# Optimization experiments

Measured on AMD Instinct MI355X. Metric: run time of the kernel, lower is better.

The kernel has to match this reference:

```python
import jax, jax.numpy as jnp
import numpy as np

# ---- configuration (matches init_kwargs) ----
CONTROL_BITS = 8
DATA_BITS = 256          # output_units
STATE_UNITS = 512        # hidden_state_dim
NUM_HEADS = 4
NUM_SHIFT = 3            # odd, required by circular conv
M = 32                   # memory content size (slots per address)
N_ADDR = 256             # memory_addresses_size
SEQ_LEN = 256
BATCH = 64
IN_DIM = CONTROL_BITS + DATA_BITS
READ_SIZE = NUM_HEADS * M
# per-head interface params: s(shift), jd(1), j(3), gamma(1), erase(M), add(M), k(M), beta(1), g(1)
PARAM_SIZES = [NUM_SHIFT, 1, 3, 1, M, M, M, 1, 1]
CUM = np.cumsum([0] + PARAM_SIZES).tolist()
HEAD_PARAM = CUM[-1]
UPDATE_SIZE = NUM_HEADS * HEAD_PARAM
COMB = IN_DIM + STATE_UNITS + READ_SIZE
EPS = 1e-12


def setup_inputs() -> dict:
    key = jax.random.key(0)
    ks = jax.random.split(key, 4)
    def lin(k, fi, fo):
        return (jax.random.normal(k, (fi, fo), jnp.float32) / np.sqrt(fi).astype(np.float32))
    return {
        "inputs": jax.random.normal(ks[0], (BATCH, SEQ_LEN, IN_DIM), jnp.float32),
        "Wo": lin(ks[1], COMB, DATA_BITS), "bo": jnp.zeros((DATA_BITS,), jnp.float32),
        "Ws": lin(ks[2], COMB, STATE_UNITS), "bs": jnp.zeros((STATE_UNITS,), jnp.float32),
        "Wu": lin(ks[3], COMB, UPDATE_SIZE), "bu": jnp.zeros((UPDATE_SIZE,), jnp.float32),
    }


def _circular_conv(x, f):
    # x: [B,H,N], f: [B,H,S] (S odd). y[i] = sum_j x[(i - S//2 + j) mod N] * f[j]
    S = f.shape[-1]
    left = S // 2
    return sum(f[..., j:j + 1] * jnp.roll(x, left - j, axis=-1) for j in range(S))


def _dwm_cell(carry, x_t, Wo, bo, Ws, bs, Wu, bu):
    state, wt, wt_dyn, mem = carry  # [B,S_u], [B,H,N], [B,H,N], [B,M,N]
    B = x_t.shape[0]

    # --- step 1: attention read:  wt [B,H,N] x mem [B,M,N] -> [B,H,M] ---
    read = jnp.einsum('bhn,bmn->bhm', wt, mem).reshape(B, READ_SIZE)

    # --- step 2: controller ---
    comb = jnp.concatenate([x_t, state, read], axis=-1)      # [B, COMB]
    new_state = jax.nn.sigmoid(comb @ Ws + bs)
    out = jax.nn.sigmoid(comb @ Wo + bo)
    upd = (comb @ Wu + bu).reshape(B, NUM_HEADS, HEAD_PARAM)

    s, jd, j, gamma, erase, add, k, beta, g = [
        upd[..., CUM[i]:CUM[i + 1]] for i in range(len(PARAM_SIZES))]
    s = jax.nn.softmax(jax.nn.softplus(s), axis=-1)          # shift weighting
    gamma = 1.0 + jax.nn.softplus(gamma)                      # sharpening >= 1
    jd = jax.nn.sigmoid(jd)                                   # snapshot gate
    j = jax.nn.softmax(j, axis=-1)                            # 3-way jump attention
    erase = jax.nn.sigmoid(erase)
    k = jnp.tanh(k)                                           # content key
    beta = jax.nn.softplus(beta)                              # key strength
    g = jax.nn.sigmoid(g)                                     # interpolation gate

    # --- step 3a: write to memory using previous head weights ---
    # erase: product over heads of (1 - e_h outer w_h); add: sum over heads
    mem = mem * jnp.prod(1.0 - erase[..., :, None] * wt[..., None, :], axis=1)
    mem = mem + jnp.einsum('bhm,bhn->bmn', add, wt)

    # --- step 3b: content addressing (cosine similarity on updated memory) ---
    k_hat = k / (jnp.linalg.norm(k, axis=-1, keepdims=True) + EPS)
    mem_hat = mem / (jnp.linalg.norm(mem, axis=-2, keepdims=True) + EPS)
    wt_c = jax.nn.softmax(beta * jnp.einsum('bhm,bmn->bhn', k_hat, mem_hat), axis=-1)
    wt_g = g * wt_c + (1.0 - g) * wt

    # --- step 3c: shift then sharpen ---
    wt_s = _circular_conv(wt_g, s)
    wt_s = (wt_s + EPS) ** gamma
    wt_s = wt_s / jnp.sum(wt_s, axis=-1, keepdims=True)

    # --- step 3d: snapshot (bookmark) update + jump mechanism ---
    wt_dyn = (1.0 - jd) * wt_dyn + jd * wt_s
    wt0 = jnp.zeros_like(wt_s).at[..., 0].set(1.0)            # fixed attention to address 0
    wt_new = j[..., 0:1] * wt_s + j[..., 1:2] * wt_dyn + j[..., 2:3] * wt0

    return (new_state, wt_new, wt_dyn, mem), out


def reference(inputs, Wo, bo, Ws, bs, Wu, bu):
    B = inputs.shape[0]
    dt = inputs.dtype
    state0 = jnp.ones((B, STATE_UNITS), dt)
    wt0 = jnp.zeros((B, NUM_HEADS, N_ADDR), dt).at[..., 0].set(1.0)
    mem0 = jnp.full((B, M, N_ADDR), 0.01, dt)

    def step(carry, x_t):
        return _dwm_cell(carry, x_t, Wo, bo, Ws, bs, Wu, bu)

    _, outs = jax.lax.scan(step, (state0, wt0, wt0, mem0), jnp.swapaxes(inputs, 0, 1))
    return jnp.swapaxes(outs, 0, 1)  # [B, SEQ_LEN, DATA_BITS]
```

## Files before the change

kernel.cpp:

```cpp
#include <hip/hip_runtime.h>
#include <hip/hip_fp16.h>
#include <math.h>


#define NHEAD 4
#define MSZ   32
#define NADDR 256
#define SEQ   256
#define INDIM 264
#define SU    512
#define DB    256
#define UPDN  424
#define COMBN 904
#define HP    106
#define MEMP  257
#define WTP   257
#define NOC   149
#define KSL   6
#define NOUT  1192

#define HWS_OFF 0
#define HWO_OFF 462848
#define HWU_OFF 694272
#define HW_TOT  1077568
#define PACK_G4 (HW_TOT / 4)

#define O_MEM    0
#define O_WT     8224
#define O_WTDYN  9252
#define O_PART   10280
#define O_COMB   17432
#define O_STATE  18336
#define O_READ   18848
#define O_UPD    18976
#define O_ERASE  19400
#define O_KHAT   19528
#define O_SHIFT  19656
#define O_JMP    19668
#define O_JD     19680
#define O_GAMMA  19684
#define O_BETA   19688
#define O_G      19692
#define O_SMAX   19696
#define O_SSUM   19700
#define O_PSUM   19704
#define SMEM_FLOATS 19708

__device__ __forceinline__ float sigmoidf_(float x) { return 1.0f / (1.0f + expf(-x)); }
__device__ __forceinline__ float softplusf_(float x) { return fmaxf(x, 0.0f) + log1pf(expf(-fabsf(x))); }

__global__ __launch_bounds__(256) void pack_w(
    const float* __restrict__ Ws, const float* __restrict__ Wo,
    const float* __restrict__ Wu, __half* __restrict__ dst)
{
    int g = blockIdx.x * 256 + threadIdx.x;
    if (g >= PACK_G4) return;
    const int T1 = HWO_OFF / 4, T2 = HWU_OFF / 4;
    const float* src; int off;
    if (g < T1)      { src = Ws; off = g * 4; }
    else if (g < T2) { src = Wo; off = (g - T1) * 4; }
    else             { src = Wu; off = (g - T2) * 4; }
    float4 v = *(const float4*)(src + off);
    __half2 a = __floats2half2_rn(v.x, v.y);
    __half2 b = __floats2half2_rn(v.z, v.w);
    *(__half2*)(dst + (size_t)g * 4)     = a;
    *(__half2*)(dst + (size_t)g * 4 + 2) = b;
}

#define FMA8(P, C) { float c_ = (C); \
    float2 f0_ = __half22float2(*(const __half2*)&(P).x); \
    float2 f1_ = __half22float2(*(const __half2*)&(P).y); \
    float2 f2_ = __half22float2(*(const __half2*)&(P).z); \
    float2 f3_ = __half22float2(*(const __half2*)&(P).w); \
    a0 = fmaf(c_, f0_.x, a0); a1 = fmaf(c_, f0_.y, a1); \
    a2 = fmaf(c_, f1_.x, a2); a3 = fmaf(c_, f1_.y, a3); \
    a4 = fmaf(c_, f2_.x, a4); a5 = fmaf(c_, f2_.y, a5); \
    a6 = fmaf(c_, f3_.x, a6); a7 = fmaf(c_, f3_.y, a7); }

__global__ __launch_bounds__(1024, 4) void dwm_kernel(
    const float* __restrict__ xin,
    const __half* __restrict__ hW,
    const float* __restrict__ bo, const float* __restrict__ bs,
    const float* __restrict__ bu,
    float* __restrict__ out)
{
    const int b = blockIdx.x;
    const int tid = threadIdx.x;

    extern __shared__ float smem[];
    float* s_mem   = smem + O_MEM;
    float* s_wt    = smem + O_WT;
    float* s_wtdyn = smem + O_WTDYN;
    float* s_part  = smem + O_PART;
    float* s_logit = smem + O_PART;
    float* s_wts   = smem + O_PART + 1028;
    float* s_comb  = smem + O_COMB;
    float* s_state = smem + O_STATE;
    float* s_read  = smem + O_READ;
    float* s_upd   = smem + O_UPD;
    float* s_erase = smem + O_ERASE;
    float* s_khat  = smem + O_KHAT;
    float* s_shift = smem + O_SHIFT;
    float* s_jmp   = smem + O_JMP;
    float* s_jd    = smem + O_JD;
    float* s_gamma = smem + O_GAMMA;
    float* s_beta  = smem + O_BETA;
    float* s_g     = smem + O_G;
    float* s_smax  = smem + O_SMAX;
    float* s_ssum  = smem + O_SSUM;
    float* s_psum  = smem + O_PSUM;

    if (tid < SU) s_state[tid] = 1.0f;
    {
        int h = tid >> 8, n = tid & 255;
        float v = (n == 0) ? 1.0f : 0.0f;
        s_wt[h * WTP + n] = v;
        s_wtdyn[h * WTP + n] = v;
    }
    for (int idx = tid; idx < MSZ * NADDR; idx += 1024) {
        int m = idx >> 8, n = idx & 255;
        s_mem[m * MEMP + n] = 0.01f;
    }
    __syncthreads();

    const int mv_ks = tid / NOC;
    const int mv_oc = tid - mv_ks * NOC;
    const bool mv_act = (mv_ks < KSL);
    const int mv_k0 = 152 * mv_ks;
    const int mv_nit = (mv_ks < 5) ? 38 : 36;
    const __half* mv_W; int mv_ncol, mv_c;
    if (mv_oc < 64)       { mv_W = hW + HWS_OFF; mv_ncol = SU;   mv_c = mv_oc * 8; }
    else if (mv_oc < 96)  { mv_W = hW + HWO_OFF; mv_ncol = DB;   mv_c = (mv_oc - 64) * 8; }
    else                  { mv_W = hW + HWU_OFF; mv_ncol = UPDN; mv_c = (mv_oc - 96) * 8; }

    for (int t = 0; t < SEQ; ++t) {
        {
            int pair = tid >> 3, sub = tid & 7;
            int h = pair >> 5, pp = pair & 31;
            int m = ((pp & 7) << 2) | (pp >> 3);
            float p = 0.0f;
            #pragma unroll 8
            for (int k = 0; k < 32; ++k) {
                int n = sub + (k << 3);
                p = fmaf(s_wt[h * WTP + n], s_mem[m * MEMP + n], p);
            }
            p += __shfl_down(p, 4);
            p += __shfl_down(p, 2);
            p += __shfl_down(p, 1);
            if (sub == 0) s_read[h * MSZ + m] = p;
        }
        __syncthreads();

        if (tid < INDIM)              s_comb[tid] = xin[((size_t)b * SEQ + t) * INDIM + tid];
        else if (tid < INDIM + SU)    s_comb[tid] = s_state[tid - INDIM];
        else if (tid < COMBN)         s_comb[tid] = s_read[tid - (INDIM + SU)];
        __syncthreads();

        if (mv_act) {
            const __half* wp = mv_W + (size_t)mv_k0 * mv_ncol + mv_c;
            const int stride = mv_ncol;
            float a0=0.f,a1=0.f,a2=0.f,a3=0.f,a4=0.f,a5=0.f,a6=0.f,a7=0.f;
            uint4 p0 = *(const uint4*)(wp);
            uint4 p1 = *(const uint4*)(wp + stride);
            uint4 p2 = *(const uint4*)(wp + 2 * stride);
            uint4 p3 = *(const uint4*)(wp + 3 * stride);
            wp += 4 * stride;
            int k = mv_k0;
            for (int it = 0; it < mv_nit - 1; ++it) {
                uint4 n0 = *(const uint4*)(wp);
                uint4 n1 = *(const uint4*)(wp + stride);
                uint4 n2 = *(const uint4*)(wp + 2 * stride);
                uint4 n3 = *(const uint4*)(wp + 3 * stride);
                wp += 4 * stride;
                float4 cb = *(const float4*)&s_comb[k];
                FMA8(p0, cb.x); FMA8(p1, cb.y); FMA8(p2, cb.z); FMA8(p3, cb.w);
                k += 4;
                p0 = n0; p1 = n1; p2 = n2; p3 = n3;
            }
            float4 cb = *(const float4*)&s_comb[k];
            FMA8(p0, cb.x); FMA8(p1, cb.y); FMA8(p2, cb.z); FMA8(p3, cb.w);
            float* dst = s_part + mv_ks * NOUT + mv_oc * 8;
            *(float4*)dst       = make_float4(a0, a1, a2, a3);
            *(float4*)(dst + 4) = make_float4(a4, a5, a6, a7);
        }
        __syncthreads();

        for (int v = tid; v < NOUT; v += 1024) {
            float s = s_part[v] + s_part[NOUT + v] + s_part[2 * NOUT + v]
                    + s_part[3 * NOUT + v] + s_part[4 * NOUT + v] + s_part[5 * NOUT + v];
            if (v < SU) {
                s_state[v] = sigmoidf_(s + bs[v]);
            } else if (v < SU + DB) {
                int c = v - SU;
                out[((size_t)b * SEQ + t) * DB + c] = sigmoidf_(s + bo[c]);
            } else {
                int c = v - (SU + DB);
                s_upd[c] = s + bu[c];
            }
        }
        __syncthreads();

        if (tid < NHEAD * MSZ) {
            int h = tid >> 5, e = tid & 31;
            const float* uu = &s_upd[h * HP];
            s_erase[h * MSZ + e] = sigmoidf_(uu[8 + e]);
            float kv = tanhf(uu[72 + e]);
            float ss = kv * kv;
            ss += __shfl_xor(ss, 1);
            ss += __shfl_xor(ss, 2);
            ss += __shfl_xor(ss, 4);
            ss += __shfl_xor(ss, 8);
            ss += __shfl_xor(ss, 16);
            s_khat[h * MSZ + e] = kv / (sqrtf(ss) + 1e-12f);
        }
        if (tid < NHEAD) {
            const float* uu = &s_upd[tid * HP];
            float a0 = softplusf_(uu[0]), a1 = softplusf_(uu[1]), a2 = softplusf_(uu[2]);
            float mx = fmaxf(a0, fmaxf(a1, a2));
            float e0 = expf(a0 - mx), e1 = expf(a1 - mx), e2 = expf(a2 - mx);
            float inv = 1.0f / (e0 + e1 + e2);
            s_shift[tid * 3 + 0] = e0 * inv;
            s_shift[tid * 3 + 1] = e1 * inv;
            s_shift[tid * 3 + 2] = e2 * inv;
            s_jd[tid] = sigmoidf_(uu[3]);
            float j0 = uu[4], j1 = uu[5], j2 = uu[6];
            float jm = fmaxf(j0, fmaxf(j1, j2));
            float f0 = expf(j0 - jm), f1 = expf(j1 - jm), f2 = expf(j2 - jm);
            float jinv = 1.0f / (f0 + f1 + f2);
            s_jmp[tid * 3 + 0] = f0 * jinv;
            s_jmp[tid * 3 + 1] = f1 * jinv;
            s_jmp[tid * 3 + 2] = f2 * jinv;
            s_gamma[tid] = 1.0f + softplusf_(uu[7]);
            s_beta[tid] = softplusf_(uu[104]);
            s_g[tid] = sigmoidf_(uu[105]);
        }
        __syncthreads();

        #pragma unroll
        for (int r = 0; r < 8; ++r) {
            int idx = tid + (r << 10);
            int m = idx >> 8, n = idx & 255;
            float w0 = s_wt[0 * WTP + n], w1 = s_wt[1 * WTP + n];
            float w2 = s_wt[2 * WTP + n], w3 = s_wt[3 * WTP + n];
            float prod = (1.0f - s_erase[0 * MSZ + m] * w0) * (1.0f - s_erase[1 * MSZ + m] * w1)
                       * (1.0f - s_erase[2 * MSZ + m] * w2) * (1.0f - s_erase[3 * MSZ + m] * w3);
            float addv = s_upd[0 * HP + 40 + m] * w0 + s_upd[1 * HP + 40 + m] * w1
                       + s_upd[2 * HP + 40 + m] * w2 + s_upd[3 * HP + 40 + m] * w3;
            s_mem[m * MEMP + n] = s_mem[m * MEMP + n] * prod + addv;
        }
        __syncthreads();

        {
            int h = tid >> 8, n = tid & 255;
            float ss = 0.0f, d = 0.0f;
            #pragma unroll 8
            for (int m = 0; m < MSZ; ++m) {
                float v = s_mem[m * MEMP + n];
                ss = fmaf(v, v, ss);
                d = fmaf(s_khat[h * MSZ + m], v, d);
            }
            s_logit[h * WTP + n] = s_beta[h] * d / (sqrtf(ss) + 1e-12f);
        }
        __syncthreads();

        if (tid < 256) {
            int h = tid >> 6, lane = tid & 63;
            float mx = -1e30f;
            #pragma unroll
            for (int k = 0; k < 4; ++k) mx = fmaxf(mx, s_logit[h * WTP + lane + (k << 6)]);
            for (int m2 = 32; m2 >= 1; m2 >>= 1) mx = fmaxf(mx, __shfl_xor(mx, m2));
            float sm = 0.0f;
            #pragma unroll
            for (int k = 0; k < 4; ++k) sm += expf(s_logit[h * WTP + lane + (k << 6)] - mx);
            for (int m2 = 32; m2 >= 1; m2 >>= 1) sm += __shfl_xor(sm, m2);
            if (lane == 0) { s_smax[h] = mx; s_ssum[h] = sm; }
        }
        __syncthreads();

        {
            int h = tid >> 8, n = tid & 255;
            float gg = s_g[h], om = 1.0f - gg;
            float inv = 1.0f / s_ssum[h], mx = s_smax[h];
            int nm = (n + 255) & 255, np = (n + 1) & 255;
            float wgm = gg * expf(s_logit[h * WTP + nm] - mx) * inv + om * s_wt[h * WTP + nm];
            float wg0 = gg * expf(s_logit[h * WTP + n ] - mx) * inv + om * s_wt[h * WTP + n ];
            float wgp = gg * expf(s_logit[h * WTP + np] - mx) * inv + om * s_wt[h * WTP + np];
            float v = s_shift[h * 3 + 0] * wgm + s_shift[h * 3 + 1] * wg0 + s_shift[h * 3 + 2] * wgp;
            s_wts[h * WTP + n] = powf(v + 1e-12f, s_gamma[h]);
        }
        __syncthreads();

        if (tid < 256) {
            int h = tid >> 6, lane = tid & 63;
            float sm = 0.0f;
            #pragma unroll
            for (int k = 0; k < 4; ++k) sm += s_wts[h * WTP + lane + (k << 6)];
            for (int m2 = 32; m2 >= 1; m2 >>= 1) sm += __shfl_xor(sm, m2);
            if (lane == 0) s_psum[h] = sm;
        }
        __syncthreads();

        {
            int h = tid >> 8, n = tid & 255;
            float ws_ = s_wts[h * WTP + n] / s_psum[h];
            float jd = s_jd[h];
            float dyn = (1.0f - jd) * s_wtdyn[h * WTP + n] + jd * ws_;
            s_wtdyn[h * WTP + n] = dyn;
            float w0v = (n == 0) ? 1.0f : 0.0f;
            s_wt[h * WTP + n] = s_jmp[h * 3 + 0] * ws_ + s_jmp[h * 3 + 1] * dyn + s_jmp[h * 3 + 2] * w0v;
        }
        __syncthreads();
    }
}

extern "C" void kernel_launch(void* const* d_in, const int* in_sizes, int n_in,
                              void* d_out, int out_size, void* d_ws, size_t ws_size,
                              hipStream_t stream) {
    const float* x  = (const float*)d_in[0];
    const float* Wo = (const float*)d_in[1];
    const float* bo = (const float*)d_in[2];
    const float* Ws = (const float*)d_in[3];
    const float* bs = (const float*)d_in[4];
    const float* Wu = (const float*)d_in[5];
    const float* bu = (const float*)d_in[6];
    float* outp = (float*)d_out;
    __half* hW = (__half*)d_ws;

    int pack_blocks = (PACK_G4 + 255) / 256;
    hipLaunchKernelGGL(pack_w, dim3(pack_blocks), dim3(256), 0, stream, Ws, Wo, Wu, hW);
    hipLaunchKernelGGL(dwm_kernel, dim3(64), dim3(1024), SMEM_FLOATS * 4, stream,
                       x, (const __half*)hW, bo, bs, bu, outp);
}
```

Before: 7.685 ms.

## Split each batch row's matvec across two cooperating blocks with flag sync

Launches 128 blocks cooperatively instead of 64, so two blocks share each batch element's controller matvec. Block 0 computes the state/output columns and block 1 computes the rest of the columns. They exchange new state and update vectors through global double-buffered scratch, using per-step atomic flags and spin-waits. This halves the per-block weight streaming and uses more CUs, at the cost of a global handshake every timestep and duplicated memory/attention work in both blocks.

```diff
diff --git a/kernel.cpp b/kernel.cpp
--- a/kernel.cpp
+++ b/kernel.cpp
@@ -15,36 +15,40 @@
 #define HP    106
 #define MEMP  257
 #define WTP   257
-#define NOC   149
-#define KSL   6
-#define NOUT  1192
+#define NOCP  75
+#define KSL2  12
+#define PNOUT 600
 
 #define HWS_OFF 0
 #define HWO_OFF 462848
 #define HWU_OFF 694272
 #define HW_TOT  1077568
 #define PACK_G4 (HW_TOT / 4)
+#define SB0_F   538784
+#define UB0_F   604320
+#define FLAG_BYTE_OFF 2634368
+#define FLAG_BYTES 16384
 
 #define O_MEM    0
 #define O_WT     8224
 #define O_WTDYN  9252
 #define O_PART   10280
-#define O_COMB   17432
-#define O_STATE  18336
-#define O_READ   18848
-#define O_UPD    18976
-#define O_ERASE  19400
-#define O_KHAT   19528
-#define O_SHIFT  19656
-#define O_JMP    19668
-#define O_JD     19680
-#define O_GAMMA  19684
-#define O_BETA   19688
-#define O_G      19692
-#define O_SMAX   19696
-#define O_SSUM   19700
-#define O_PSUM   19704
-#define SMEM_FLOATS 19708
+#define O_COMB   17480
+#define O_STATE  18384
+#define O_READ   18896
+#define O_UPD    19024
+#define O_ERASE  19448
+#define O_KHAT   19576
+#define O_SHIFT  19704
+#define O_JMP    19716
+#define O_JD     19728
+#define O_GAMMA  19732
+#define O_BETA   19736
+#define O_G      19740
+#define O_SMAX   19744
+#define O_SSUM   19748
+#define O_PSUM   19752
+#define SMEM_FLOATS 19756
 
 __device__ __forceinline__ float sigmoidf_(float x) { return 1.0f / (1.0f + expf(-x)); }
 __device__ __forceinline__ float softplusf_(float x) { return fmaxf(x, 0.0f) + log1pf(expf(-fabsf(x))); }
@@ -82,10 +86,20 @@
     const __half* __restrict__ hW,
     const float* __restrict__ bo, const float* __restrict__ bs,
     const float* __restrict__ bu,
-    float* __restrict__ out)
+    float* __restrict__ out,
+    float* __restrict__ sbuf,
+    float* __restrict__ ubuf,
+    unsigned* __restrict__ flags)
 {
-    const int b = blockIdx.x;
+    const int blk = blockIdx.x;
+    const int b = blk & 63;
+    const int s = blk >> 6;
     const int tid = threadIdx.x;
+
+    unsigned* sflag = flags;
+    unsigned* uflag = flags + 64 * 32;
+    unsigned* myflag = (s ? uflag : sflag) + b * 32;
+    unsigned* wflag  = (s ? sflag : uflag) + b * 32;
 
     extern __shared__ float smem[];
     float* s_mem   = smem + O_MEM;
@@ -123,36 +137,41 @@
     }
     __syncthreads();
 
-    const int mv_ks = tid / NOC;
-    const int mv_oc = tid - mv_ks * NOC;
-    const bool mv_act = (mv_ks < KSL);
-    const int mv_k0 = 152 * mv_ks;
-    const int mv_nit = (mv_ks < 5) ? 38 : 36;
+    const int mv_ks  = tid / NOCP;
+    const int mv_ocl = tid - mv_ks * NOCP;
+    const int mv_ocg = s * 75 + mv_ocl;
+    const bool mv_act = (mv_ks < KSL2) && (mv_ocg < 149);
+    const int mv_k0  = (mv_ks < 10) ? 76 * mv_ks : 760 + 72 * (mv_ks - 10);
+    const int mv_nit = (mv_ks < 10) ? 19 : 18;
     const __half* mv_W; int mv_ncol, mv_c;
-    if (mv_oc < 64)       { mv_W = hW + HWS_OFF; mv_ncol = SU;   mv_c = mv_oc * 8; }
-    else if (mv_oc < 96)  { mv_W = hW + HWO_OFF; mv_ncol = DB;   mv_c = (mv_oc - 64) * 8; }
-    else                  { mv_W = hW + HWU_OFF; mv_ncol = UPDN; mv_c = (mv_oc - 96) * 8; }
+    if (mv_ocg < 64)      { mv_W = hW + HWS_OFF; mv_ncol = SU;   mv_c = mv_ocg * 8; }
+    else if (mv_ocg < 96) { mv_W = hW + HWO_OFF; mv_ncol = DB;   mv_c = (mv_ocg - 64) * 8; }
+    else                  { mv_W = hW + HWU_OFF; mv_ncol = UPDN; mv_c = (mv_ocg - 96) * 8; }
+
+    const int NOUTs = PNOUT - s * 8;
 
     for (int t = 0; t < SEQ; ++t) {
+        const int p = t & 1;
+
         {
             int pair = tid >> 3, sub = tid & 7;
             int h = pair >> 5, pp = pair & 31;
             int m = ((pp & 7) << 2) | (pp >> 3);
-            float p = 0.0f;
+            float pv = 0.0f;
             #pragma unroll 8
             for (int k = 0; k < 32; ++k) {
                 int n = sub + (k << 3);
-                p = fmaf(s_wt[h * WTP + n], s_mem[m * MEMP + n], p);
+                pv = fmaf(s_wt[h * WTP + n], s_mem[m * MEMP + n], pv);
             }
-            p += __shfl_down(p, 4);
-            p += __shfl_down(p, 2);
-            p += __shfl_down(p, 1);
-            if (sub == 0) s_read[h * MSZ + m] = p;
+            pv += __shfl_down(pv, 4);
+            pv += __shfl_down(pv, 2);
+            pv += __shfl_down(pv, 1);
+            if (sub == 0) s_read[h * MSZ + m] = pv;
         }
         __syncthreads();
 
         if (tid < INDIM)              s_comb[tid] = xin[((size_t)b * SEQ + t) * INDIM + tid];
-        else if (tid < INDIM + SU)    s_comb[tid] = s_state[tid - INDIM];
+        else if (tid < INDIM + SU)    s_comb[tid] = (t == 0) ? 1.0f : s_state[tid - INDIM];
         else if (tid < COMBN)         s_comb[tid] = s_read[tid - (INDIM + SU)];
         __syncthreads();
 
@@ -179,25 +198,45 @@
             }
             float4 cb = *(const float4*)&s_comb[k];
             FMA8(p0, cb.x); FMA8(p1, cb.y); FMA8(p2, cb.z); FMA8(p3, cb.w);
-            float* dst = s_part + mv_ks * NOUT + mv_oc * 8;
+            float* dst = s_part + mv_ks * PNOUT + mv_ocl * 8;
             *(float4*)dst       = make_float4(a0, a1, a2, a3);
             *(float4*)(dst + 4) = make_float4(a4, a5, a6, a7);
         }
         __syncthreads();
 
-        for (int v = tid; v < NOUT; v += 1024) {
-            float s = s_part[v] + s_part[NOUT + v] + s_part[2 * NOUT + v]
-                    + s_part[3 * NOUT + v] + s_part[4 * NOUT + v] + s_part[5 * NOUT + v];
-            if (v < SU) {
-                s_state[v] = sigmoidf_(s + bs[v]);
-            } else if (v < SU + DB) {
-                int c = v - SU;
-                out[((size_t)b * SEQ + t) * DB + c] = sigmoidf_(s + bo[c]);
+        if (tid < NOUTs) {
+            float sm = 0.0f;
+            #pragma unroll
+            for (int ks = 0; ks < KSL2; ++ks) sm += s_part[ks * PNOUT + tid];
+            int vg = s * PNOUT + tid;
+            if (vg < SU) {
+                float val = sigmoidf_(sm + bs[vg]);
+                s_state[vg] = val;
+                sbuf[((size_t)p * 64 + b) * SU + vg] = val;
+            } else if (vg < SU + DB) {
+                int c = vg - SU;
+                out[((size_t)b * SEQ + t) * DB + c] = sigmoidf_(sm + bo[c]);
             } else {
-                int c = v - (SU + DB);
-                s_upd[c] = s + bu[c];
+                int c = vg - (SU + DB);
+                float val = sm + bu[c];
+                s_upd[c] = val;
+                ubuf[((size_t)p * 64 + b) * UPDN + c] = val;
             }
         }
+        __syncthreads();
+
+        if (t == SEQ - 1) break;
+
+        if (tid == 0) {
+            __threadfence();
+            atomicExch(myflag, (unsigned)(t + 1));
+            while (atomicAdd(wflag, 0u) < (unsigned)(t + 1))
+                __builtin_amdgcn_s_sleep(2);
+            __threadfence();
+        }
+        __syncthreads();
+        if (s == 0) { if (tid < UPDN) s_upd[tid]   = ubuf[((size_t)p * 64 + b) * UPDN + tid]; }
+        else        { if (tid < SU)   s_state[tid] = sbuf[((size_t)p * 64 + b) * SU + tid]; }
         __syncthreads();
 
         if (tid < NHEAD * MSZ) {
@@ -325,9 +364,16 @@
     const float* bu = (const float*)d_in[6];
     float* outp = (float*)d_out;
     __half* hW = (__half*)d_ws;
-
+    float* sbuf = (float*)d_ws + SB0_F;
+    float* ubuf = (float*)d_ws + UB0_F;
+    unsigned* flags = (unsigned*)((char*)d_ws + FLAG_BYTE_OFF);
+
+    hipMemsetAsync((char*)d_ws + FLAG_BYTE_OFF, 0, FLAG_BYTES, stream);
     int pack_blocks = (PACK_G4 + 255) / 256;
     hipLaunchKernelGGL(pack_w, dim3(pack_blocks), dim3(256), 0, stream, Ws, Wo, Wu, hW);
-    hipLaunchKernelGGL(dwm_kernel, dim3(64), dim3(1024), SMEM_FLOATS * 4, stream,
-                       x, (const __half*)hW, bo, bs, bu, outp);
+
+    void* args[] = { (void*)&x, (void*)&hW, (void*)&bo, (void*)&bs, (void*)&bu,
+                     (void*)&outp, (void*)&sbuf, (void*)&ubuf, (void*)&flags };
+    hipLaunchCooperativeKernel((const void*)dwm_kernel, dim3(128), dim3(1024),
+                               args, SMEM_FLOATS * 4, stream);
 }
```

Measured after the change: 7.740 ms. Within noise of the previous version (+0.7%).
